# Optimization experiments

Measured on AMD Instinct MI355X. Metric: run time of the kernel, lower is better.

## Reference

```python
import jax, jax.numpy as jnp
import numpy as np

WIN = 7
K1, K2 = 0.01, 0.03
NP_ = WIN ** 3
COV_NORM = NP_ / (NP_ - 1)


def _box3d(x, win=WIN):
    # Separable box filter: three 1D VALID convs (same math as the dense
    for ax in range(3):
        kshape = [1, 1, 1, 1, 1]
        kshape[2 + ax] = win
        k = jnp.ones(kshape, x.dtype) / win
        x = jax.lax.conv_general_dilated(
            x, k, window_strides=(1, 1, 1), padding='VALID',
            dimension_numbers=('NCDHW', 'OIDHW', 'NCDHW'))
    return x


def setup_inputs() -> dict:
    key = jax.random.key(0)
    k1, k2 = jax.random.split(key)
    B, C, D, H, W = 4, 1, 128, 128, 128
    X = jax.random.normal(k1, (B, C, D, H, W), dtype=jnp.float32)
    Y = jax.random.normal(k2, (B, C, D, H, W), dtype=jnp.float32)
    data_range = jnp.ones((B, 1, 1, 1, 1), dtype=jnp.float32)
    return {"X": X, "Y": Y, "data_range": data_range}


def reference(X, Y, data_range):
    C1 = (K1 * data_range) ** 2
    C2 = (K2 * data_range) ** 2
    ux = _box3d(X)
    uy = _box3d(Y)
    uxx = _box3d(X * X)
    uyy = _box3d(Y * Y)
    uxy = _box3d(X * Y)
    vx = COV_NORM * (uxx - ux * ux)
    vy = COV_NORM * (uyy - uy * uy)
    vxy = COV_NORM * (uxy - ux * uy)
    A1 = 2 * ux * uy + C1
    A2 = 2 * vxy + C2
    B1 = ux ** 2 + uy ** 2 + C1
    B2 = vx + vy + C2
    S = (A1 * A2) / (B1 * B2)
    return S.mean()
```

## Files before the change

### kernel.cpp

```cpp
#include <hip/hip_runtime.h>

#define NFULL 128
#define NOUT  122

#define S1_R 34
#define S1_Q 748
#define S1_B 3740
#define NBLK 1024

__device__ __forceinline__ void phaseA_task(const float* __restrict__ px,
                                            const float* __restrict__ py,
                                            float* __restrict__ s1p)
{
    float xs[8], ys[8];
#pragma unroll
    for (int k = 0; k < 4; ++k) {
        float2 tx = *(const float2*)(px + 2 * k);
        float2 ty = *(const float2*)(py + 2 * k);
        xs[2 * k] = tx.x; xs[2 * k + 1] = tx.y;
        ys[2 * k] = ty.x; ys[2 * k + 1] = ty.y;
    }
    float sx = 0.f, sy = 0.f, sxx = 0.f, syy = 0.f, sxy = 0.f;
#pragma unroll
    for (int k = 0; k < 7; ++k) {
        sx += xs[k]; sy += ys[k];
        sxx = fmaf(xs[k], xs[k], sxx);
        syy = fmaf(ys[k], ys[k], syy);
        sxy = fmaf(xs[k], ys[k], sxy);
    }
    float tx2 = sx - xs[0] + xs[7];
    float ty2 = sy - ys[0] + ys[7];
    float txx = sxx - xs[0] * xs[0] + xs[7] * xs[7];
    float tyy = syy - ys[0] * ys[0] + ys[7] * ys[7];
    float txy = sxy - xs[0] * ys[0] + xs[7] * ys[7];
    *(float2*)(s1p + 0 * S1_Q) = make_float2(sx,  tx2);
    *(float2*)(s1p + 1 * S1_Q) = make_float2(sy,  ty2);
    *(float2*)(s1p + 2 * S1_Q) = make_float2(sxx, txx);
    *(float2*)(s1p + 3 * S1_Q) = make_float2(syy, tyy);
    *(float2*)(s1p + 4 * S1_Q) = make_float2(sxy, txy);
}

__global__ __launch_bounds__(256, 4)
void ssim3d_kernel(const float* __restrict__ X, const float* __restrict__ Y,
                   const float* __restrict__ DR, double* __restrict__ ws, int mode)
{
    __shared__ __align__(16) float s1[2 * S1_B];

    const int tid = threadIdx.x;
    int bi = blockIdx.x;
    const int bb = bi & 3;  bi >>= 2;
    const int ht = bi & 7;  bi >>= 3;
    const int wt = bi & 3;  bi >>= 2;
    const int dc = bi;

    const int h0 = ht << 4;
    const int w0 = (wt == 3) ? 90 : (wt << 5);
    const int w_hi = (wt == 3) ? 122 : ((wt == 2) ? 90 : (w0 + 32));
    const int csize = (dc < 2) ? 16 : 15;
    const int d0 = (dc < 2) ? (dc << 4) : (32 + (dc - 2) * 15);
    const int nsl = csize + 6;

    const float dr = DR[bb];
    const float c1s = (0.01f * dr) * (0.01f * dr) * 117649.0f;
    const float c2s = (0.03f * dr) * (0.03f * dr) * 117649.0f;
    const float tni = 1.0f / 343.0f;
    const float kkA = 2.0f * 117649.0f / 342.0f;
    const float kkB = 117649.0f / 342.0f;

    const int sA  = tid & 15;
    const int rA0 = tid >> 4;
    const int rA1 = 16 + (tid >> 4);
    int grA0 = h0 + rA0; if (grA0 > NFULL - 1) grA0 = NFULL - 1;
    int grA1 = h0 + rA1; if (grA1 > NFULL - 1) grA1 = NFULL - 1;
    const int coffA = w0 + 2 * sA;

    const int sC = tid & 15, hC = tid >> 4;
    const int gh  = h0 + hC;
    const int gw0 = w0 + 2 * sC;
    const bool vh = (gh < NOUT);
    const bool vld0 = vh && (gw0 < w_hi);
    const bool vld1 = vh && (gw0 + 1 < w_hi);

    const size_t planeStride = (size_t)NFULL * NFULL;
    const size_t bbase = (size_t)bb * NFULL * planeStride;

    float2 ring[7][5];
    float2 run[5];
#pragma unroll
    for (int k = 0; k < 7; ++k)
#pragma unroll
        for (int q = 0; q < 5; ++q) ring[k][q] = make_float2(0.f, 0.f);
#pragma unroll
    for (int q = 0; q < 5; ++q) run[q] = make_float2(0.f, 0.f);
    float acc = 0.0f;

    for (int base = 0; base <= nsl; base += 7) {
#pragma unroll
        for (int u = 0; u < 7; ++u) {
            const int s = base + u;
            if (s <= nsl) {
                if (s < nsl) {
                    float* dst = s1 + (size_t)((s & 1) * S1_B);
                    const int dIn = d0 + s;
                    const float* Xp = X + bbase + (size_t)dIn * planeStride;
                    const float* Yp = Y + bbase + (size_t)dIn * planeStride;
                    phaseA_task(Xp + grA0 * NFULL + coffA, Yp + grA0 * NFULL + coffA,
                                dst + rA0 * S1_R + 2 * sA);
                    if (tid < 96)
                        phaseA_task(Xp + grA1 * NFULL + coffA, Yp + grA1 * NFULL + coffA,
                                    dst + rA1 * S1_R + 2 * sA);
                }
                if (s >= 1) {
                    const float* src = s1 + (size_t)(((s - 1) & 1) * S1_B)
                                          + hC * S1_R + 2 * sC;
                    const int slot = (u + 6) % 7;
#pragma unroll
                    for (int q = 0; q < 5; ++q) {
                        const float* p = src + q * S1_Q;
                        float2 h = *(const float2*)p;
#pragma unroll
                        for (int r = 1; r < 7; ++r) {
                            float2 v = *(const float2*)(p + r * S1_R);
                            h.x += v.x; h.y += v.y;
                        }
                        run[q].x += h.x - ring[slot][q].x;
                        run[q].y += h.y - ring[slot][q].y;
                        ring[slot][q] = h;
                    }
                    if (s >= 7) {
#pragma unroll
                        for (int j = 0; j < 2; ++j) {
                            const bool vld = j ? vld1 : vld0;
                            if (vld) {
                                float Sx  = j ? run[0].y : run[0].x;
                                float Sy  = j ? run[1].y : run[1].x;
                                float Sxx = j ? run[2].y : run[2].x;
                                float Syy = j ? run[3].y : run[3].x;
                                float Sxy = j ? run[4].y : run[4].x;
                                float P = Sx * Sy;
                                float Q = fmaf(Sx, Sx, Sy * Sy);
                                float A1 = fmaf(2.f, P, c1s);
                                float A2 = fmaf(kkA, fmaf(-tni, P, Sxy), c2s);
                                float B1 = Q + c1s;
                                float B2 = fmaf(kkB, fmaf(-tni, Q, Sxx + Syy), c2s);
                                float num = A1 * A2;
                                float den = B1 * B2;
                                float r0 = __builtin_amdgcn_rcpf(den);
                                r0 = r0 * fmaf(-den, r0, 2.0f);
                                acc = fmaf(num, r0, acc);
                            }
                        }
                    }
                }
                __syncthreads();
            }
        }
    }

#pragma unroll
    for (int off = 32; off; off >>= 1) acc += __shfl_down(acc, off);
    if ((tid & 63) == 0) s1[tid >> 6] = acc;
    __syncthreads();
    if (tid == 0) {
        double t = (double)s1[0] + (double)s1[1] + (double)s1[2] + (double)s1[3];
        if (mode) ws[blockIdx.x] = t;
        else      atomicAdd(ws, t);
    }
}

__global__ void ssim3d_finalize(const double* __restrict__ ws, float* __restrict__ out, int mode)
{
    if (mode) {
        __shared__ double sm[4];
        const int tid = threadIdx.x;
        double t = 0.0;
        for (int i = tid; i < NBLK; i += 256) t += ws[i];
#pragma unroll
        for (int off = 32; off; off >>= 1) t += __shfl_down(t, off);
        if ((tid & 63) == 0) sm[tid >> 6] = t;
        __syncthreads();
        if (tid == 0) {
            double r = sm[0] + sm[1] + sm[2] + sm[3];
            out[0] = (float)(r * (1.0 / 7263392.0));
        }
    } else {
        if (threadIdx.x == 0)
            out[0] = (float)(ws[0] * (1.0 / 7263392.0));
    }
}

extern "C" void kernel_launch(void* const* d_in, const int* in_sizes, int n_in,
                              void* d_out, int out_size, void* d_ws, size_t ws_size,
                              hipStream_t stream)
{
    const float* X  = (const float*)d_in[0];
    const float* Y  = (const float*)d_in[1];
    const float* DR = (const float*)d_in[2];
    double* ws = (double*)d_ws;

    const int mode = (ws_size >= NBLK * sizeof(double)) ? 1 : 0;
    if (!mode) hipMemsetAsync(d_ws, 0, sizeof(double), stream);
    ssim3d_kernel<<<NBLK, 256, 0, stream>>>(X, Y, DR, ws, mode);
    ssim3d_finalize<<<1, 256, 0, stream>>>(ws, (float*)d_out, mode);
}
```

Before: 124.0 us.

## Add sliding-window H-pass stage through shared memory and deepen depth chunks

Measured after the change: 126.9 us. 1.02x slower.

```diff
diff --git a/kernel.cpp b/kernel.cpp
--- a/kernel.cpp
+++ b/kernel.cpp
@@ -6,7 +6,10 @@
 #define S1_R 34
 #define S1_Q 748
 #define S1_B 3740
-#define NBLK 1024
+#define S2_R 34
+#define S2_Q 544
+#define S2_B 2720
+#define NBLK 768
 
 __device__ __forceinline__ void phaseA_task(const float* __restrict__ px,
                                             const float* __restrict__ py,
@@ -40,11 +43,12 @@
     *(float2*)(s1p + 4 * S1_Q) = make_float2(sxy, txy);
 }
 
-__global__ __launch_bounds__(256, 4)
+__global__ __launch_bounds__(256, 3)
 void ssim3d_kernel(const float* __restrict__ X, const float* __restrict__ Y,
                    const float* __restrict__ DR, double* __restrict__ ws, int mode)
 {
     __shared__ __align__(16) float s1[2 * S1_B];
+    __shared__ __align__(16) float s2[2 * S2_B];
 
     const int tid = threadIdx.x;
     int bi = blockIdx.x;
@@ -56,8 +60,8 @@
     const int h0 = ht << 4;
     const int w0 = (wt == 3) ? 90 : (wt << 5);
     const int w_hi = (wt == 3) ? 122 : ((wt == 2) ? 90 : (w0 + 32));
-    const int csize = (dc < 2) ? 16 : 15;
-    const int d0 = (dc < 2) ? (dc << 4) : (32 + (dc - 2) * 15);
+    const int csize = (dc < 2) ? 21 : 20;
+    const int d0 = (dc < 2) ? dc * 21 : (42 + (dc - 2) * 20);
     const int nsl = csize + 6;
 
     const float dr = DR[bb];
@@ -94,13 +98,13 @@
     for (int q = 0; q < 5; ++q) run[q] = make_float2(0.f, 0.f);
     float acc = 0.0f;
 
-    for (int base = 0; base <= nsl; base += 7) {
+    for (int base = 0; base <= nsl + 1; base += 7) {
 #pragma unroll
         for (int u = 0; u < 7; ++u) {
             const int s = base + u;
-            if (s <= nsl) {
+            if (s <= nsl + 1) {
                 if (s < nsl) {
-                    float* dst = s1 + (size_t)((s & 1) * S1_B);
+                    float* dst = s1 + (s & 1) * S1_B;
                     const int dIn = d0 + s;
                     const float* Xp = X + bbase + (size_t)dIn * planeStride;
                     const float* Yp = Y + bbase + (size_t)dIn * planeStride;
@@ -110,24 +114,50 @@
                         phaseA_task(Xp + grA1 * NFULL + coffA, Yp + grA1 * NFULL + coffA,
                                     dst + rA1 * S1_R + 2 * sA);
                 }
-                if (s >= 1) {
-                    const float* src = s1 + (size_t)(((s - 1) & 1) * S1_B)
-                                          + hC * S1_R + 2 * sC;
-                    const int slot = (u + 6) % 7;
+                if (s >= 1 && s <= nsl) {
+                    const float* sb = s1 + ((s - 1) & 1) * S1_B;
+                    float*       db = s2 + ((s - 1) & 1) * S2_B;
+#pragma unroll
+                    for (int rep = 0; rep < 2; ++rep) {
+                        const int t = rep ? (256 + tid) : tid;
+                        if (rep == 0 || tid < 64) {
+                            const int sB  = t & 15;
+                            const int tq  = t >> 4;
+                            const int qB  = tq % 5;
+                            const int r0  = (tq / 5) << 2;
+                            const float* src = sb + qB * S1_Q + 2 * sB;
+                            float*       dst = db + qB * S2_Q + 2 * sB;
+                            float2 v[10];
+#pragma unroll
+                            for (int r = 0; r < 10; ++r)
+                                v[r] = *(const float2*)(src + (r0 + r) * S1_R);
+                            float ax = v[0].x, ay = v[0].y;
+#pragma unroll
+                            for (int r = 1; r < 7; ++r) { ax += v[r].x; ay += v[r].y; }
+                            *(float2*)(dst + r0 * S2_R) = make_float2(ax, ay);
+#pragma unroll
+                            for (int i = 1; i < 4; ++i) {
+                                ax += v[6 + i].x - v[i - 1].x;
+                                ay += v[6 + i].y - v[i - 1].y;
+                                *(float2*)(dst + (r0 + i) * S2_R) = make_float2(ax, ay);
+                            }
+                        }
+                    }
+                }
+                if (s >= 2) {
+                    const float* src = s2 + ((s - 2) & 1) * S2_B + hC * S2_R + 2 * sC;
+                    const int slot = (u + 5) % 7;
+                    float2 p[5];
+#pragma unroll
+                    for (int q = 0; q < 5; ++q)
+                        p[q] = *(const float2*)(src + q * S2_Q);
 #pragma unroll
                     for (int q = 0; q < 5; ++q) {
-                        const float* p = src + q * S1_Q;
-                        float2 h = *(const float2*)p;
-#pragma unroll
-                        for (int r = 1; r < 7; ++r) {
-                            float2 v = *(const float2*)(p + r * S1_R);
-                            h.x += v.x; h.y += v.y;
-                        }
-                        run[q].x += h.x - ring[slot][q].x;
-                        run[q].y += h.y - ring[slot][q].y;
-                        ring[slot][q] = h;
+                        run[q].x += p[q].x - ring[slot][q].x;
+                        run[q].y += p[q].y - ring[slot][q].y;
+                        ring[slot][q] = p[q];
                     }
-                    if (s >= 7) {
+                    if (s >= 8) {
 #pragma unroll
                         for (int j = 0; j < 2; ++j) {
                             const bool vld = j ? vld1 : vld0;
```

## Make each wave own a private LDS tile and drop block-wide barriers

Applied to the files above, without the earlier changes.

Result: slower. 132.3 us (+6.7%).

```diff
diff --git a/kernel.cpp b/kernel.cpp
--- a/kernel.cpp
+++ b/kernel.cpp
@@ -2,15 +2,18 @@
 
 #define NFULL 128
 #define NOUT  122
-
-#define S1_R 34
-#define S1_Q 748
-#define S1_B 3740
-#define NBLK 1024
-
-__device__ __forceinline__ void phaseA_task(const float* __restrict__ px,
-                                            const float* __restrict__ py,
-                                            float* __restrict__ s1p)
+#define NBLK  1024
+
+#define WS_R 18
+#define WS_Q 252
+#define HS_R 18
+#define HS_Q 144
+#define HS_OFF 1260
+#define WAVE_LDS 1984
+
+__device__ __forceinline__ void wsum_task(const float* __restrict__ px,
+                                          const float* __restrict__ py,
+                                          float* __restrict__ wsp)
 {
     float xs[8], ys[8];
 #pragma unroll
@@ -33,53 +36,66 @@
     float txx = sxx - xs[0] * xs[0] + xs[7] * xs[7];
     float tyy = syy - ys[0] * ys[0] + ys[7] * ys[7];
     float txy = sxy - xs[0] * ys[0] + xs[7] * ys[7];
-    *(float2*)(s1p + 0 * S1_Q) = make_float2(sx,  tx2);
-    *(float2*)(s1p + 1 * S1_Q) = make_float2(sy,  ty2);
-    *(float2*)(s1p + 2 * S1_Q) = make_float2(sxx, txx);
-    *(float2*)(s1p + 3 * S1_Q) = make_float2(syy, tyy);
-    *(float2*)(s1p + 4 * S1_Q) = make_float2(sxy, txy);
+    *(float2*)(wsp + 0 * WS_Q) = make_float2(sx,  tx2);
+    *(float2*)(wsp + 1 * WS_Q) = make_float2(sy,  ty2);
+    *(float2*)(wsp + 2 * WS_Q) = make_float2(sxx, txx);
+    *(float2*)(wsp + 3 * WS_Q) = make_float2(syy, tyy);
+    *(float2*)(wsp + 4 * WS_Q) = make_float2(sxy, txy);
 }
 
 __global__ __launch_bounds__(256, 4)
 void ssim3d_kernel(const float* __restrict__ X, const float* __restrict__ Y,
-                   const float* __restrict__ DR, double* __restrict__ ws, int mode)
-{
-    __shared__ __align__(16) float s1[2 * S1_B];
-
-    const int tid = threadIdx.x;
+                   const float* __restrict__ DR, double* __restrict__ wsout, int mode)
+{
+    __shared__ __align__(16) float lds[4 * WAVE_LDS];
+
+    const int tid  = threadIdx.x;
+    const int wave = tid >> 6;
+    const int lane = tid & 63;
+    const int c = lane & 7;
+    const int g = lane >> 3;
+
     int bi = blockIdx.x;
     const int bb = bi & 3;  bi >>= 2;
-    const int ht = bi & 7;  bi >>= 3;
-    const int wt = bi & 3;  bi >>= 2;
+    const int ht = bi & 3;  bi >>= 2;
+    const int wt = bi & 7;  bi >>= 3;
     const int dc = bi;
 
-    const int h0 = ht << 4;
-    const int w0 = (wt == 3) ? 90 : (wt << 5);
-    const int w_hi = (wt == 3) ? 122 : ((wt == 2) ? 90 : (w0 + 32));
+    const int hbase = ht * 32 + wave * 8;
+    const int w0 = wt * 16;
     const int csize = (dc < 2) ? 16 : 15;
     const int d0 = (dc < 2) ? (dc << 4) : (32 + (dc - 2) * 15);
     const int nsl = csize + 6;
 
-    const float dr = DR[bb];
+    const float dr  = DR[bb];
     const float c1s = (0.01f * dr) * (0.01f * dr) * 117649.0f;
     const float c2s = (0.03f * dr) * (0.03f * dr) * 117649.0f;
     const float tni = 1.0f / 343.0f;
     const float kkA = 2.0f * 117649.0f / 342.0f;
     const float kkB = 117649.0f / 342.0f;
 
-    const int sA  = tid & 15;
-    const int rA0 = tid >> 4;
-    const int rA1 = 16 + (tid >> 4);
-    int grA0 = h0 + rA0; if (grA0 > NFULL - 1) grA0 = NFULL - 1;
-    int grA1 = h0 + rA1; if (grA1 > NFULL - 1) grA1 = NFULL - 1;
-    const int coffA = w0 + 2 * sA;
-
-    const int sC = tid & 15, hC = tid >> 4;
-    const int gh  = h0 + hC;
-    const int gw0 = w0 + 2 * sC;
-    const bool vh = (gh < NOUT);
-    const bool vld0 = vh && (gw0 < w_hi);
-    const bool vld1 = vh && (gw0 + 1 < w_hi);
+    float* wsb = lds + wave * WAVE_LDS;
+    float* hsb = wsb + HS_OFF;
+
+    int grow0 = hbase + g;      if (grow0 > NFULL - 1) grow0 = NFULL - 1;
+    int grow1 = hbase + g + 8;  if (grow1 > NFULL - 1) grow1 = NFULL - 1;
+    const bool hasA1 = (g < 6);
+    int colb = w0 + 2 * c; if (colb > NFULL - 8) colb = NFULL - 8;
+    float* wsp0 = wsb + g * WS_R + 2 * c;
+    float* wsp1 = wsb + (g + 8) * WS_R + 2 * c;
+
+    const bool actB = (lane < 40);
+    const int cB = lane & 7;
+    const int qB = lane >> 3;
+    const float* srcB = wsb + qB * WS_Q + 2 * cB;
+    float*       dstB = hsb + qB * HS_Q + 2 * cB;
+
+    const float* srcC = hsb + g * HS_R + 2 * c;
+    const int gh  = hbase + g;
+    const int gw0 = w0 + 2 * c;
+    const bool vh   = (gh < NOUT);
+    const bool vld0 = vh && (gw0 < NOUT);
+    const bool vld1 = vh && (gw0 + 1 < NOUT);
 
     const size_t planeStride = (size_t)NFULL * NFULL;
     const size_t bbase = (size_t)bb * NFULL * planeStride;
@@ -94,40 +110,49 @@
     for (int q = 0; q < 5; ++q) run[q] = make_float2(0.f, 0.f);
     float acc = 0.0f;
 
-    for (int base = 0; base <= nsl; base += 7) {
+    for (int base = 0; base < nsl; base += 7) {
 #pragma unroll
         for (int u = 0; u < 7; ++u) {
             const int s = base + u;
-            if (s <= nsl) {
-                if (s < nsl) {
-                    float* dst = s1 + (size_t)((s & 1) * S1_B);
-                    const int dIn = d0 + s;
-                    const float* Xp = X + bbase + (size_t)dIn * planeStride;
-                    const float* Yp = Y + bbase + (size_t)dIn * planeStride;
-                    phaseA_task(Xp + grA0 * NFULL + coffA, Yp + grA0 * NFULL + coffA,
-                                dst + rA0 * S1_R + 2 * sA);
-                    if (tid < 96)
-                        phaseA_task(Xp + grA1 * NFULL + coffA, Yp + grA1 * NFULL + coffA,
-                                    dst + rA1 * S1_R + 2 * sA);
+            if (s < nsl) {
+                const int dIn = d0 + s;
+                const float* Xp = X + bbase + (size_t)dIn * planeStride;
+                const float* Yp = Y + bbase + (size_t)dIn * planeStride;
+
+                wsum_task(Xp + grow0 * NFULL + colb, Yp + grow0 * NFULL + colb, wsp0);
+                if (hasA1)
+                    wsum_task(Xp + grow1 * NFULL + colb, Yp + grow1 * NFULL + colb, wsp1);
+
+                if (actB) {
+                    float2 v[14];
+#pragma unroll
+                    for (int r = 0; r < 14; ++r)
+                        v[r] = *(const float2*)(srcB + r * WS_R);
+                    float ax = v[0].x, ay = v[0].y;
+#pragma unroll
+                    for (int r = 1; r < 7; ++r) { ax += v[r].x; ay += v[r].y; }
+                    *(float2*)(dstB + 0 * HS_R) = make_float2(ax, ay);
+#pragma unroll
+                    for (int i = 1; i < 8; ++i) {
+                        ax += v[6 + i].x - v[i - 1].x;
+                        ay += v[6 + i].y - v[i - 1].y;
+                        *(float2*)(dstB + i * HS_R) = make_float2(ax, ay);
+                    }
                 }
-                if (s >= 1) {
-                    const float* src = s1 + (size_t)(((s - 1) & 1) * S1_B)
-                                          + hC * S1_R + 2 * sC;
-                    const int slot = (u + 6) % 7;
+
+                {
+                    const int slot = u;
+                    float2 p[5];
+#pragma unroll
+                    for (int q = 0; q < 5; ++q)
+                        p[q] = *(const float2*)(srcC + q * HS_Q);
 #pragma unroll
                     for (int q = 0; q < 5; ++q) {
-                        const float* p = src + q * S1_Q;
-                        float2 h = *(const float2*)p;
-#pragma unroll
-                        for (int r = 1; r < 7; ++r) {
-                            float2 v = *(const float2*)(p + r * S1_R);
-                            h.x += v.x; h.y += v.y;
-                        }
-                        run[q].x += h.x - ring[slot][q].x;
-                        run[q].y += h.y - ring[slot][q].y;
-                        ring[slot][q] = h;
+                        run[q].x += p[q].x - ring[slot][q].x;
+                        run[q].y += p[q].y - ring[slot][q].y;
+                        ring[slot][q] = p[q];
                     }
-                    if (s >= 7) {
+                    if (s >= 6) {
 #pragma unroll
                         for (int j = 0; j < 2; ++j) {
                             const bool vld = j ? vld1 : vld0;
@@ -152,19 +177,19 @@
                         }
                     }
                 }
-                __syncthreads();
             }
         }
     }
 
 #pragma unroll
     for (int off = 32; off; off >>= 1) acc += __shfl_down(acc, off);
-    if ((tid & 63) == 0) s1[tid >> 6] = acc;
+    __syncthreads();
+    if (lane == 0) lds[wave] = acc;
     __syncthreads();
     if (tid == 0) {
-        double t = (double)s1[0] + (double)s1[1] + (double)s1[2] + (double)s1[3];
-        if (mode) ws[blockIdx.x] = t;
-        else      atomicAdd(ws, t);
+        double t = (double)lds[0] + (double)lds[1] + (double)lds[2] + (double)lds[3];
+        if (mode) wsout[blockIdx.x] = t;
+        else      atomicAdd(wsout, t);
     }
 }
 
```
